# Optimization experiments

Hardware: AMD Instinct MI355X
Metric: run time of the kernel (lower is better)

## Reference

```python
import jax, jax.numpy as jnp
import numpy as np


def setup_inputs() -> dict:
    key = jax.random.key(0)
    ks = jax.random.split(key, 9)
    B, LAT, OBS, HID = 4096, 128, 64, 1024
    s = 0.05  # keep tanh out of full saturation
    return {
        "z": jax.random.normal(ks[0], (B, LAT), jnp.float32),
        "W_l2h": jax.random.normal(ks[1], (HID, LAT), jnp.float32) * s,
        "b_l2h": jax.random.normal(ks[2], (HID,), jnp.float32) * s,
        "W_ih": jax.random.normal(ks[3], (HID, OBS), jnp.float32) * s,
        "b_ih": jax.random.normal(ks[4], (HID,), jnp.float32) * s,
        "W_hh": jax.random.normal(ks[5], (HID, HID), jnp.float32) * s,
        "b_hh": jax.random.normal(ks[6], (HID,), jnp.float32) * s,
        "W_ho": jax.random.normal(ks[7], (OBS, HID), jnp.float32) * s,
        "b_ho": jax.random.normal(ks[8], (OBS,), jnp.float32) * s,
        "seq_len": 70,
    }


def reference(z, W_l2h, b_l2h, W_ih, b_ih, W_hh, b_hh, W_ho, b_ho, seq_len):
    B = z.shape[0]
    obs_dim = W_ho.shape[0]
    # latent -> initial hidden state (nn.Linear)
    h0 = z @ W_l2h.T + b_l2h                         # [B, HID]
    x0 = jnp.zeros((B, obs_dim), dtype=z.dtype)      # first RNN input is zeros

    def step(carry, _):
        h, x = carry
        # tanh RNN cell: h' = tanh(x W_ih^T + b_ih + h W_hh^T + b_hh)
        h = jnp.tanh(x @ W_ih.T + b_ih + h @ W_hh.T + b_hh)
        y = h @ W_ho.T + b_ho                        # output projection [B, OBS]
        x_next = jax.lax.stop_gradient(y)
        return (h, x_next), y

    _, ys = jax.lax.scan(step, (h0, x0), None, length=seq_len)  # [T, B, OBS]
    return jnp.transpose(ys, (1, 0, 2))              # [B, T, OBS]
```

## Files before the change

### kernel.cpp

```cpp
#include <hip/hip_runtime.h>
#include <hip/hip_bf16.h>
#include <stdint.h>

typedef _Float16 f16;
typedef _Float16 f16x8 __attribute__((ext_vector_type(8)));
typedef float f32x4 __attribute__((ext_vector_type(4)));

#define B_SZ 4096
#define HID  1024
#define LAT  128
#define OBS  64
#define TSEQ 70
#define SPLIT_SCALE 2048.0f
#define SPLIT_INV   (1.0f / 2048.0f)

__device__ __forceinline__ size_t tidx(int row, int k, int K) {
  return (size_t)((row >> 4) * (K >> 5) + (k >> 5)) * 512
       + ((k >> 3) & 3) * 128 + (row & 15) * 8 + (k & 7);
}

__device__ __forceinline__ void gl2lds16(const void* g, void* l) {
  __builtin_amdgcn_global_load_lds(
      (const __attribute__((address_space(1))) void*)g,
      (__attribute__((address_space(3))) void*)l, 16, 0, 0);
}

__device__ __forceinline__ float tanh_fast(float x) {
  float e = __expf(2.0f * x);
  return 1.0f - 2.0f / (e + 1.0f);
}

__global__ __launch_bounds__(256, 2) void rnn_step_split(
    const f16* __restrict__ Ah, const f16* __restrict__ Al,
    const f16* __restrict__ Wh, const f16* __restrict__ Wl,
    const float* __restrict__ bias,
    f16* __restrict__ Hh, f16* __restrict__ Hl, int K)
{
  __shared__ __align__(16) f16 ring[3][24 * 512];

  const int lane = threadIdx.x & 63;
  const int wave = threadIdx.x >> 6;
  const int bm = blockIdx.x;
  const int bn = blockIdx.y;
  const int lo8 = lane * 8;
  const int kc = K >> 5;

  f32x4 acc0[2][4], acc1[2][4];
  const f32x4 z4 = {0.f, 0.f, 0.f, 0.f};
#pragma unroll
  for (int i = 0; i < 2; ++i)
#pragma unroll
    for (int j = 0; j < 4; ++j) { acc0[i][j] = z4; acc1[i][j] = z4; }

  auto stage = [&](int it, int slot) {
    f16* b = ring[slot];
#pragma unroll
    for (int u = 0; u < 2; ++u) {
      const int rg = wave * 2 + u;
      const size_t ga = (size_t)((bm * 8 + rg) * kc + it) * 512 + lo8;
      gl2lds16(Ah + ga, b + rg * 512);
      gl2lds16(Al + ga, b + (8 + rg) * 512);
    }
    const size_t gw = (size_t)((bn * 4 + wave) * kc + it) * 512 + lo8;
    gl2lds16(Wh + gw, b + (16 + wave) * 512);
    gl2lds16(Wl + gw, b + (20 + wave) * 512);
  };

  auto compute = [&](int slot) {
    const f16* b = ring[slot];
    f16x8 vah[2], val[2], vwh[4], vwl[4];
#pragma unroll
    for (int i = 0; i < 2; ++i) {
      vah[i] = *(const f16x8*)&b[(wave * 2 + i) * 512 + lo8];
      val[i] = *(const f16x8*)&b[(8 + wave * 2 + i) * 512 + lo8];
    }
#pragma unroll
    for (int j = 0; j < 4; ++j) {
      vwh[j] = *(const f16x8*)&b[(16 + j) * 512 + lo8];
      vwl[j] = *(const f16x8*)&b[(20 + j) * 512 + lo8];
    }
#pragma unroll
    for (int i = 0; i < 2; ++i)
#pragma unroll
      for (int j = 0; j < 4; ++j) {
        acc0[i][j] = __builtin_amdgcn_mfma_f32_16x16x32_f16(vah[i], vwh[j], acc0[i][j], 0, 0, 0);
        acc1[i][j] = __builtin_amdgcn_mfma_f32_16x16x32_f16(vah[i], vwl[j], acc1[i][j], 0, 0, 0);
        acc1[i][j] = __builtin_amdgcn_mfma_f32_16x16x32_f16(val[i], vwh[j], acc1[i][j], 0, 0, 0);
      }
  };

  stage(0, 0);
  int cur = 0;
  for (int it = 0; it + 1 < kc; ++it) {
    const int nxt = (cur == 2) ? 0 : cur + 1;
    stage(it + 1, nxt);
    asm volatile("s_waitcnt vmcnt(6)" ::: "memory");
    __builtin_amdgcn_s_barrier();
    compute(cur);
    cur = nxt;
  }
  asm volatile("s_waitcnt vmcnt(0)" ::: "memory");
  __builtin_amdgcn_s_barrier();
  compute(cur);

  const int rq = lane >> 4;
  const int cl = lane & 15;
#pragma unroll
  for (int j = 0; j < 4; ++j) {
    const int gcol = bn * 64 + j * 16 + cl;
    const float bb = bias[gcol];
#pragma unroll
    for (int i = 0; i < 2; ++i) {
      const int grow = bm * 128 + wave * 32 + i * 16 + rq * 4;
#pragma unroll
      for (int r = 0; r < 4; ++r) {
        const float a = acc0[i][j][r] + acc1[i][j][r] * SPLIT_INV + bb;
        const float t = tanh_fast(a);
        const f16 hi = (f16)t;
        const size_t idx = tidx(grow + r, gcol, HID);
        Hh[idx] = hi;
        Hl[idx] = (f16)((t - (float)hi) * SPLIT_SCALE);
      }
    }
  }
}

__global__ __launch_bounds__(256, 2) void proj_kernel(
    const f16* __restrict__ H, const f16* __restrict__ Who,
    const float* __restrict__ bho, float* __restrict__ Y, int t0)
{
  __shared__ __align__(16) f16 As[128 * 64];
  __shared__ __align__(16) f16 Bs[64 * 64];
  const int lane = threadIdx.x & 63;
  const int wave = threadIdx.x >> 6;
  const int bm = blockIdx.x;
  const int lo8 = lane * 8;

  f32x4 acc[2][4];
  const f32x4 z4 = {0.f, 0.f, 0.f, 0.f};
#pragma unroll
  for (int i = 0; i < 2; ++i)
#pragma unroll
    for (int j = 0; j < 4; ++j) acc[i][j] = z4;

  for (int kt = 0; kt < HID; kt += 64) {
    const int kch = kt >> 5;
#pragma unroll
    for (int u = 0; u < 4; ++u) {
      const int cidx = wave * 4 + u;
      const int mt = cidx >> 1, s = cidx & 1;
      gl2lds16(H + (size_t)((bm * 8 + mt) * 32 + kch + s) * 512 + lo8, &As[cidx * 512]);
    }
#pragma unroll
    for (int u = 0; u < 2; ++u) {
      const int cidx = wave * 2 + u;
      const int nt = cidx >> 1, s = cidx & 1;
      gl2lds16(Who + (size_t)(nt * 32 + kch + s) * 512 + lo8, &Bs[cidx * 512]);
    }
    __syncthreads();
#pragma unroll
    for (int s = 0; s < 2; ++s) {
      f16x8 af[2], bfr[4];
#pragma unroll
      for (int i = 0; i < 2; ++i)
        af[i] = *(const f16x8*)&As[(((wave * 2 + i) << 1) | s) * 512 + lo8];
#pragma unroll
      for (int j = 0; j < 4; ++j)
        bfr[j] = *(const f16x8*)&Bs[((j << 1) | s) * 512 + lo8];
#pragma unroll
      for (int i = 0; i < 2; ++i)
#pragma unroll
        for (int j = 0; j < 4; ++j)
          acc[i][j] = __builtin_amdgcn_mfma_f32_16x16x32_f16(af[i], bfr[j], acc[i][j], 0, 0, 0);
    }
    __syncthreads();
  }

  const int rq = lane >> 4;
  const int cl = lane & 15;
#pragma unroll
  for (int j = 0; j < 4; ++j) {
    const int col = j * 16 + cl;
    const float bb = bho[col];
#pragma unroll
    for (int i = 0; i < 2; ++i)
#pragma unroll
      for (int r = 0; r < 4; ++r) {
        const int row = bm * 128 + wave * 32 + i * 16 + rq * 4 + r;
        const int t = t0 + (row >> 12);
        const int b = row & 4095;
        Y[((size_t)b * TSEQ + t) * OBS + col] = acc[i][j][r] + bb;
      }
  }
}

__global__ void cast_tiled_kernel(const float* __restrict__ x, f16* __restrict__ y,
                                  int K, int n) {
  int i = blockIdx.x * blockDim.x + threadIdx.x;
  if (i < n) y[tidx(i / K, i % K, K)] = (f16)x[i];
}

__global__ void split_tiled_kernel(const float* __restrict__ x, f16* __restrict__ hi,
                                   f16* __restrict__ lo, int K, int n) {
  int i = blockIdx.x * blockDim.x + threadIdx.x;
  if (i < n) {
    float v = x[i];
    f16 h = (f16)v;
    size_t o = tidx(i / K, i % K, K);
    hi[o] = h;
    lo[o] = (f16)((v - (float)h) * SPLIT_SCALE);
  }
}

__global__ void prep_weff(const float* __restrict__ Whh, const float* __restrict__ Wih,
                          const float* __restrict__ Who,
                          f16* __restrict__ Wh, f16* __restrict__ Wl) {
  const int n = blockIdx.x;
  __shared__ float wih_row[OBS];
  if (threadIdx.x < OBS) wih_row[threadIdx.x] = Wih[n * OBS + threadIdx.x];
  __syncthreads();
  for (int k = threadIdx.x; k < HID; k += 256) {
    float s = Whh[(size_t)n * HID + k];
#pragma unroll 8
    for (int o = 0; o < OBS; ++o) s = fmaf(wih_row[o], Who[(size_t)o * HID + k], s);
    const size_t idx = tidx(n, k, HID);
    f16 h = (f16)s;
    Wh[idx] = h;
    Wl[idx] = (f16)((s - (float)h) * SPLIT_SCALE);
  }
}

__global__ void prep_w1(const float* __restrict__ Whh, const float* __restrict__ Wl2h,
                        f16* __restrict__ W1h, f16* __restrict__ W1l) {
  const int n = blockIdx.x, j = threadIdx.x;
  float s = 0.f;
  for (int k = 0; k < HID; ++k) s = fmaf(Whh[(size_t)n * HID + k], Wl2h[(size_t)k * LAT + j], s);
  const size_t idx = tidx(n, j, LAT);
  f16 h = (f16)s;
  W1h[idx] = h;
  W1l[idx] = (f16)((s - (float)h) * SPLIT_SCALE);
}

__global__ void prep_bias(const float* __restrict__ bih, const float* __restrict__ bhh,
                          const float* __restrict__ bho, const float* __restrict__ Wih,
                          const float* __restrict__ Whh, const float* __restrict__ bl2h,
                          float* __restrict__ beff, float* __restrict__ b1) {
  const int n = blockIdx.x, l = threadIdx.x;
  float s1 = Wih[(size_t)n * OBS + l] * bho[l];
  float s2 = 0.f;
  for (int k = l; k < HID; k += 64) s2 = fmaf(Whh[(size_t)n * HID + k], bl2h[k], s2);
#pragma unroll
  for (int off = 32; off > 0; off >>= 1) {
    s1 += __shfl_down(s1, off);
    s2 += __shfl_down(s2, off);
  }
  if (l == 0) {
    const float base = bih[n] + bhh[n];
    beff[n] = base + s1;
    b1[n]   = base + s2;
  }
}

extern "C" void kernel_launch(void* const* d_in, const int* in_sizes, int n_in,
                              void* d_out, int out_size, void* d_ws, size_t ws_size,
                              hipStream_t stream) {
  (void)in_sizes; (void)n_in; (void)out_size; (void)ws_size;
  const float* z    = (const float*)d_in[0];
  const float* Wl2h = (const float*)d_in[1];
  const float* bl2h = (const float*)d_in[2];
  const float* Wih  = (const float*)d_in[3];
  const float* bih  = (const float*)d_in[4];
  const float* Whh  = (const float*)d_in[5];
  const float* bhh  = (const float*)d_in[6];
  const float* Who  = (const float*)d_in[7];
  const float* bho  = (const float*)d_in[8];
  float* Y = (float*)d_out;

  char* ws = (char*)d_ws;
  size_t off = 0;
  auto take = [&](size_t bytes) {
    char* p = ws + off;
    off = (off + bytes + 255) & ~(size_t)255;
    return p;
  };
  f16*   Weffh = (f16*)take((size_t)HID * HID * 2);
  f16*   Weffl = (f16*)take((size_t)HID * HID * 2);
  f16*   W1h   = (f16*)take((size_t)HID * LAT * 2);
  f16*   W1l   = (f16*)take((size_t)HID * LAT * 2);
  f16*   Whob  = (f16*)take((size_t)OBS * HID * 2);
  f16*   zh    = (f16*)take((size_t)B_SZ * LAT * 2);
  f16*   zl    = (f16*)take((size_t)B_SZ * LAT * 2);
  float* beff  = (float*)take(HID * 4);
  float* b1    = (float*)take(HID * 4);

  const size_t S = (size_t)B_SZ * HID;
  f16* Hlo  = (f16*)take(2 * S * 2);
  f16* ring = (f16*)take(8 * S * 2);

  split_tiled_kernel<<<(B_SZ * LAT) / 256, 256, 0, stream>>>(z, zh, zl, LAT, B_SZ * LAT);
  cast_tiled_kernel<<<(OBS * HID) / 256, 256, 0, stream>>>(Who, Whob, HID, OBS * HID);
  prep_weff<<<HID, 256, 0, stream>>>(Whh, Wih, Who, Weffh, Weffl);
  prep_w1<<<HID, LAT, 0, stream>>>(Whh, Wl2h, W1h, W1l);
  prep_bias<<<HID, 64, 0, stream>>>(bih, bhh, bho, Wih, Whh, bl2h, beff, b1);

  dim3 sgrid(B_SZ / 128, HID / 64);
  rnn_step_split<<<sgrid, 256, 0, stream>>>(zh, zl, W1h, W1l, b1, ring, Hlo, LAT);
  for (int t = 1; t < TSEQ; ++t) {
    if ((t & 7) == 0)
      proj_kernel<<<(8 * B_SZ) / 128, 256, 0, stream>>>(ring, Whob, bho, Y, t - 8);
    rnn_step_split<<<sgrid, 256, 0, stream>>>(
        ring + (size_t)((t - 1) & 7) * S, Hlo + (size_t)((t - 1) & 1) * S,
        Weffh, Weffl, beff,
        ring + (size_t)(t & 7) * S, Hlo + (size_t)(t & 1) * S, HID);
  }
  proj_kernel<<<(6 * B_SZ) / 128, 256, 0, stream>>>(ring, Whob, bho, Y, 64);
}
```

Measured before the change: 2.180 ms.

## Load A fragments directly into registers, stage only weights through LDS ring

```diff
diff --git a/kernel.cpp b/kernel.cpp
--- a/kernel.cpp
+++ b/kernel.cpp
@@ -36,7 +36,7 @@
     const float* __restrict__ bias,
     f16* __restrict__ Hh, f16* __restrict__ Hl, int K)
 {
-  __shared__ __align__(16) f16 ring[3][24 * 512];
+  __shared__ __align__(16) f16 ringW[3][8 * 512];
 
   const int lane = threadIdx.x & 63;
   const int wave = threadIdx.x >> 6;
@@ -52,56 +52,74 @@
 #pragma unroll
     for (int j = 0; j < 4; ++j) { acc0[i][j] = z4; acc1[i][j] = z4; }
 
-  auto stage = [&](int it, int slot) {
-    f16* b = ring[slot];
-#pragma unroll
-    for (int u = 0; u < 2; ++u) {
-      const int rg = wave * 2 + u;
-      const size_t ga = (size_t)((bm * 8 + rg) * kc + it) * 512 + lo8;
-      gl2lds16(Ah + ga, b + rg * 512);
-      gl2lds16(Al + ga, b + (8 + rg) * 512);
+  const size_t aRow0 = (size_t)(bm * 8 + wave * 2) * kc;
+  const size_t aRow1 = aRow0 + kc;
+
+  struct ABuf { f16x8 h0, h1, l0, l1; };
+  auto loadA = [&](int it, ABuf& A) {
+    A.h0 = *(const f16x8*)(Ah + (aRow0 + it) * 512 + lo8);
+    A.l0 = *(const f16x8*)(Al + (aRow0 + it) * 512 + lo8);
+    A.h1 = *(const f16x8*)(Ah + (aRow1 + it) * 512 + lo8);
+    A.l1 = *(const f16x8*)(Al + (aRow1 + it) * 512 + lo8);
+  };
+
+  auto stageW = [&](int it, int slot) {
+    f16* b = ringW[slot];
+    const size_t gw = (size_t)((bn * 4 + wave) * kc + it) * 512 + lo8;
+    gl2lds16(Wh + gw, b + wave * 512);
+    gl2lds16(Wl + gw, b + (4 + wave) * 512);
+  };
+
+  auto compute = [&](int slot, const ABuf& A) {
+    const f16* b = ringW[slot];
+    f16x8 vwh[4], vwl[4];
+#pragma unroll
+    for (int j = 0; j < 4; ++j) {
+      vwh[j] = *(const f16x8*)&b[j * 512 + lo8];
+      vwl[j] = *(const f16x8*)&b[(4 + j) * 512 + lo8];
     }
-    const size_t gw = (size_t)((bn * 4 + wave) * kc + it) * 512 + lo8;
-    gl2lds16(Wh + gw, b + (16 + wave) * 512);
-    gl2lds16(Wl + gw, b + (20 + wave) * 512);
-  };
-
-  auto compute = [&](int slot) {
-    const f16* b = ring[slot];
-    f16x8 vah[2], val[2], vwh[4], vwl[4];
-#pragma unroll
-    for (int i = 0; i < 2; ++i) {
-      vah[i] = *(const f16x8*)&b[(wave * 2 + i) * 512 + lo8];
-      val[i] = *(const f16x8*)&b[(8 + wave * 2 + i) * 512 + lo8];
+#pragma unroll
+    for (int j = 0; j < 4; ++j) {
+      acc0[0][j] = __builtin_amdgcn_mfma_f32_16x16x32_f16(A.h0, vwh[j], acc0[0][j], 0, 0, 0);
+      acc1[0][j] = __builtin_amdgcn_mfma_f32_16x16x32_f16(A.h0, vwl[j], acc1[0][j], 0, 0, 0);
+      acc1[0][j] = __builtin_amdgcn_mfma_f32_16x16x32_f16(A.l0, vwh[j], acc1[0][j], 0, 0, 0);
+      acc0[1][j] = __builtin_amdgcn_mfma_f32_16x16x32_f16(A.h1, vwh[j], acc0[1][j], 0, 0, 0);
+      acc1[1][j] = __builtin_amdgcn_mfma_f32_16x16x32_f16(A.h1, vwl[j], acc1[1][j], 0, 0, 0);
+      acc1[1][j] = __builtin_amdgcn_mfma_f32_16x16x32_f16(A.l1, vwh[j], acc1[1][j], 0, 0, 0);
     }
-#pragma unroll
-    for (int j = 0; j < 4; ++j) {
-      vwh[j] = *(const f16x8*)&b[(16 + j) * 512 + lo8];
-      vwl[j] = *(const f16x8*)&b[(20 + j) * 512 + lo8];
-    }
-#pragma unroll
-    for (int i = 0; i < 2; ++i)
-#pragma unroll
-      for (int j = 0; j < 4; ++j) {
-        acc0[i][j] = __builtin_amdgcn_mfma_f32_16x16x32_f16(vah[i], vwh[j], acc0[i][j], 0, 0, 0);
-        acc1[i][j] = __builtin_amdgcn_mfma_f32_16x16x32_f16(vah[i], vwl[j], acc1[i][j], 0, 0, 0);
-        acc1[i][j] = __builtin_amdgcn_mfma_f32_16x16x32_f16(val[i], vwh[j], acc1[i][j], 0, 0, 0);
-      }
-  };
-
-  stage(0, 0);
-  int cur = 0;
-  for (int it = 0; it + 1 < kc; ++it) {
-    const int nxt = (cur == 2) ? 0 : cur + 1;
-    stage(it + 1, nxt);
+  };
+
+  ABuf A0, A1;
+  loadA(0, A0);
+  stageW(0, 0);
+  int s0 = 0;
+  int it = 0;
+  for (; it + 2 < kc; it += 2) {
+    const int s1 = (s0 == 2) ? 0 : s0 + 1;
+    const int s2 = (s1 == 2) ? 0 : s1 + 1;
+    loadA(it + 1, A1);
+    stageW(it + 1, s1);
     asm volatile("s_waitcnt vmcnt(6)" ::: "memory");
     __builtin_amdgcn_s_barrier();
-    compute(cur);
-    cur = nxt;
-  }
-  asm volatile("s_waitcnt vmcnt(0)" ::: "memory");
-  __builtin_amdgcn_s_barrier();
-  compute(cur);
+    compute(s0, A0);
+    loadA(it + 2, A0);
+    stageW(it + 2, s2);
+    asm volatile("s_waitcnt vmcnt(6)" ::: "memory");
+    __builtin_amdgcn_s_barrier();
+    compute(s1, A1);
+    s0 = s2;
+  }
+  {
+    const int s1 = (s0 == 2) ? 0 : s0 + 1;
+    loadA(kc - 1, A1);
+    stageW(kc - 1, s1);
+    asm volatile("s_waitcnt vmcnt(6)" ::: "memory");
+    __builtin_amdgcn_s_barrier();
+    compute(s0, A0);
+    asm volatile("s_waitcnt vmcnt(0)" ::: "memory");
+    __builtin_amdgcn_s_barrier();
+    compute(s1, A1);
+  }
 
   const int rq = lane >> 4;
   const int cl = lane & 15;
@@ -129,12 +147,12 @@
     const f16* __restrict__ H, const f16* __restrict__ Who,
     const float* __restrict__ bho, float* __restrict__ Y, int t0)
 {
-  __shared__ __align__(16) f16 As[128 * 64];
-  __shared__ __align__(16) f16 Bs[64 * 64];
+  __shared__ __align__(16) f16 ringB[3][4 * 512];
   const int lane = threadIdx.x & 63;
   const int wave = threadIdx.x >> 6;
   const int bm = blockIdx.x;
   const int lo8 = lane * 8;
+  const int kc = HID >> 5;
 
   f32x4 acc[2][4];
   const f32x4 z4 = {0.f, 0.f, 0.f, 0.f};
@@ -143,37 +161,59 @@
 #pragma unroll
     for (int j = 0; j < 4; ++j) acc[i][j] = z4;
 
-  for (int kt = 0; kt < HID; kt += 64) {
-    const int kch = kt >> 5;
-#pragma unroll
-    for (int u = 0; u < 4; ++u) {
-      const int cidx = wave * 4 + u;
-      const int mt = cidx >> 1, s = cidx & 1;
-      gl2lds16(H + (size_t)((bm * 8 + mt) * 32 + kch + s) * 512 + lo8, &As[cidx * 512]);
+  const size_t aRow0 = (size_t)(bm * 8 + wave * 2) * kc;
+  const size_t aRow1 = aRow0 + kc;
+
+  struct ABuf { f16x8 a0, a1; };
+  auto loadA = [&](int it, ABuf& A) {
+    A.a0 = *(const f16x8*)(H + (aRow0 + it) * 512 + lo8);
+    A.a1 = *(const f16x8*)(H + (aRow1 + it) * 512 + lo8);
+  };
+  auto stageB = [&](int it, int slot) {
+    gl2lds16(Who + (size_t)(wave * kc + it) * 512 + lo8, ringB[slot] + wave * 512);
+  };
+  auto compute = [&](int slot, const ABuf& A) {
+    const f16* b = ringB[slot];
+    f16x8 bf[4];
+#pragma unroll
+    for (int j = 0; j < 4; ++j) bf[j] = *(const f16x8*)&b[j * 512 + lo8];
+#pragma unroll
+    for (int j = 0; j < 4; ++j) {
+      acc[0][j] = __builtin_amdgcn_mfma_f32_16x16x32_f16(A.a0, bf[j], acc[0][j], 0, 0, 0);
+      acc[1][j] = __builtin_amdgcn_mfma_f32_16x16x32_f16(A.a1, bf[j], acc[1][j], 0, 0, 0);
     }
-#pragma unroll
-    for (int u = 0; u < 2; ++u) {
-      const int cidx = wave * 2 + u;
-      const int nt = cidx >> 1, s = cidx & 1;
-      gl2lds16(Who + (size_t)(nt * 32 + kch + s) * 512 + lo8, &Bs[cidx * 512]);
-    }
-    __syncthreads();
-#pragma unroll
-    for (int s = 0; s < 2; ++s) {
-      f16x8 af[2], bfr[4];
-#pragma unroll
-      for (int i = 0; i < 2; ++i)
-        af[i] = *(const f16x8*)&As[(((wave * 2 + i) << 1) | s) * 512 + lo8];
-#pragma unroll
-      for (int j = 0; j < 4; ++j)
-        bfr[j] = *(const f16x8*)&Bs[((j << 1) | s) * 512 + lo8];
-#pragma unroll
-      for (int i = 0; i < 2; ++i)
-#pragma unroll
-        for (int j = 0; j < 4; ++j)
-          acc[i][j] = __builtin_amdgcn_mfma_f32_16x16x32_f16(af[i], bfr[j], acc[i][j], 0, 0, 0);
-    }
-    __syncthreads();
+  };
+
+  ABuf A0, A1;
+  loadA(0, A0);
+  stageB(0, 0);
+  int s0 = 0;
+  int it = 0;
+  for (; it + 2 < kc; it += 2) {
+    const int s1 = (s0 == 2) ? 0 : s0 + 1;
+    const int s2 = (s1 == 2) ? 0 : s1 + 1;
+    loadA(it + 1, A1);
+    stageB(it + 1, s1);
+    asm volatile("s_waitcnt vmcnt(3)" ::: "memory");
+    __builtin_amdgcn_s_barrier();
+    compute(s0, A0);
+    loadA(it + 2, A0);
+    stageB(it + 2, s2);
+    asm volatile("s_waitcnt vmcnt(3)" ::: "memory");
+    __builtin_amdgcn_s_barrier();
+    compute(s1, A1);
+    s0 = s2;
+  }
+  {
+    const int s1 = (s0 == 2) ? 0 : s0 + 1;
+    loadA(kc - 1, A1);
+    stageB(kc - 1, s1);
+    asm volatile("s_waitcnt vmcnt(3)" ::: "memory");
+    __builtin_amdgcn_s_barrier();
+    compute(s0, A0);
+    asm volatile("s_waitcnt vmcnt(0)" ::: "memory");
+    __builtin_amdgcn_s_barrier();
+    compute(s1, A1);
   }
 
   const int rq = lane >> 4;
```

Measured after the change: 2.373 ms. 1.09x slower.

## Add weight-resident LDS kernel for recurrent steps with 512x32 tiles

Applied to the files above, without the earlier changes.

```diff
diff --git a/kernel.cpp b/kernel.cpp
--- a/kernel.cpp
+++ b/kernel.cpp
@@ -28,6 +28,102 @@
 __device__ __forceinline__ float tanh_fast(float x) {
   float e = __expf(2.0f * x);
   return 1.0f - 2.0f / (e + 1.0f);
+}
+
+__global__ __launch_bounds__(256, 1) void rnn_step_wres(
+    const f16* __restrict__ Ah, const f16* __restrict__ Al,
+    const f16* __restrict__ Wh, const f16* __restrict__ Wl,
+    const float* __restrict__ bias,
+    f16* __restrict__ Hh, f16* __restrict__ Hl)
+{
+  extern __shared__ __align__(16) f16 sW[];
+  const int lane = threadIdx.x & 63;
+  const int wave = threadIdx.x >> 6;
+  const int rb = blockIdx.x & 7;
+  const int cb = blockIdx.x >> 3;
+  const int lo8 = lane * 8;
+  const int kcA = 32;
+
+#pragma unroll
+  for (int u = 0; u < 32; ++u) {
+    const int g = wave * 32 + u;
+    const f16* src = (g < 64) ? Wh : Wl;
+    const int nrg = (g & 63) >> 5, kcid = g & 31;
+    gl2lds16(src + ((size_t)((cb * 2 + nrg) * 32 + kcid)) * 512 + lo8,
+             sW + g * 512);
+  }
+
+  f32x4 acc0[8][2], acc1[8][2];
+  const f32x4 z4 = {0.f, 0.f, 0.f, 0.f};
+#pragma unroll
+  for (int r = 0; r < 8; ++r)
+#pragma unroll
+    for (int j = 0; j < 2; ++j) { acc0[r][j] = z4; acc1[r][j] = z4; }
+
+  const int rgbase = rb * 32 + wave * 8;
+
+  struct ABuf { f16x8 h[8], l[8]; };
+  auto loadA = [&](int it, ABuf& A) {
+#pragma unroll
+    for (int r = 0; r < 8; ++r) {
+      const size_t ga = ((size_t)(rgbase + r) * kcA + it) * 512 + lo8;
+      A.h[r] = *(const f16x8*)(Ah + ga);
+      A.l[r] = *(const f16x8*)(Al + ga);
+    }
+  };
+
+  auto compute = [&](int it, const ABuf& A) {
+    f16x8 vwh[2], vwl[2];
+#pragma unroll
+    for (int j = 0; j < 2; ++j) {
+      vwh[j] = *(const f16x8*)&sW[(j * 32 + it) * 512 + lo8];
+      vwl[j] = *(const f16x8*)&sW[(64 + j * 32 + it) * 512 + lo8];
+    }
+#pragma unroll
+    for (int r = 0; r < 8; ++r)
+#pragma unroll
+      for (int j = 0; j < 2; ++j) {
+        acc0[r][j] = __builtin_amdgcn_mfma_f32_16x16x32_f16(A.h[r], vwh[j], acc0[r][j], 0, 0, 0);
+        acc1[r][j] = __builtin_amdgcn_mfma_f32_16x16x32_f16(A.h[r], vwl[j], acc1[r][j], 0, 0, 0);
+        acc1[r][j] = __builtin_amdgcn_mfma_f32_16x16x32_f16(A.l[r], vwh[j], acc1[r][j], 0, 0, 0);
+      }
+  };
+
+  ABuf A0, A1;
+  loadA(0, A0);
+  __syncthreads();
+
+  int it = 0;
+  for (; it + 2 < kcA; it += 2) {
+    loadA(it + 1, A1);
+    compute(it, A0);
+    loadA(it + 2, A0);
+    compute(it + 1, A1);
+  }
+  loadA(kcA - 1, A1);
+  compute(kcA - 2, A0);
+  compute(kcA - 1, A1);
+
+  const int rq = lane >> 4;
+  const int cl = lane & 15;
+#pragma unroll
+  for (int j = 0; j < 2; ++j) {
+    const int gcol = cb * 32 + j * 16 + cl;
+    const float bb = bias[gcol];
+#pragma unroll
+    for (int r = 0; r < 8; ++r) {
+      const int grow = rb * 512 + wave * 128 + r * 16 + rq * 4;
+#pragma unroll
+      for (int rr = 0; rr < 4; ++rr) {
+        const float a = acc0[r][j][rr] + acc1[r][j][rr] * SPLIT_INV + bb;
+        const float t = tanh_fast(a);
+        const f16 hi = (f16)t;
+        const size_t idx = tidx(grow + rr, gcol, HID);
+        Hh[idx] = hi;
+        Hl[idx] = (f16)((t - (float)hi) * SPLIT_SCALE);
+      }
+    }
+  }
 }
 
 __global__ __launch_bounds__(256, 2) void rnn_step_split(
@@ -275,6 +371,13 @@
   const float* Who  = (const float*)d_in[7];
   const float* bho  = (const float*)d_in[8];
   float* Y = (float*)d_out;
+
+  static bool configured = false;
+  if (!configured) {
+    hipFuncSetAttribute(reinterpret_cast<const void*>(rnn_step_wres),
+                        hipFuncAttributeMaxDynamicSharedMemorySize, 131072);
+    configured = true;
+  }
 
   char* ws = (char*)d_ws;
   size_t off = 0;
@@ -308,10 +411,10 @@
   for (int t = 1; t < TSEQ; ++t) {
     if ((t & 7) == 0)
       proj_kernel<<<(8 * B_SZ) / 128, 256, 0, stream>>>(ring, Whob, bho, Y, t - 8);
-    rnn_step_split<<<sgrid, 256, 0, stream>>>(
+    rnn_step_wres<<<256, 256, 131072, stream>>>(
         ring + (size_t)((t - 1) & 7) * S, Hlo + (size_t)((t - 1) & 1) * S,
         Weffh, Weffl, beff,
-        ring + (size_t)(t & 7) * S, Hlo + (size_t)(t & 1) * S, HID);
+        ring + (size_t)(t & 7) * S, Hlo + (size_t)(t & 1) * S);
   }
   proj_kernel<<<(6 * B_SZ) / 128, 256, 0, stream>>>(ring, Whob, bho, Y, 64);
 }
```

Measured after the change: 5.951 ms. +173.0%, slower.

## Fuse output projection of previous step into the recurrent step kernel

Applied to the files above, without the earlier changes.

```diff
diff --git a/kernel.cpp b/kernel.cpp
--- a/kernel.cpp
+++ b/kernel.cpp
@@ -34,9 +34,11 @@
     const f16* __restrict__ Ah, const f16* __restrict__ Al,
     const f16* __restrict__ Wh, const f16* __restrict__ Wl,
     const float* __restrict__ bias,
-    f16* __restrict__ Hh, f16* __restrict__ Hl, int K)
+    f16* __restrict__ Hh, f16* __restrict__ Hl, int K,
+    const f16* __restrict__ Who, const float* __restrict__ bho,
+    float* __restrict__ Y, int t_prev)
 {
-  __shared__ __align__(16) f16 ring[3][24 * 512];
+  __shared__ __align__(16) f16 ring[3][25 * 512];
 
   const int lane = threadIdx.x & 63;
   const int wave = threadIdx.x >> 6;
@@ -44,13 +46,16 @@
   const int bn = blockIdx.y;
   const int lo8 = lane * 8;
   const int kc = K >> 5;
-
-  f32x4 acc0[2][4], acc1[2][4];
+  const bool doproj = (t_prev >= 0) && (bn < 4);
+
+  f32x4 acc0[2][4], acc1[2][4], accy[2];
   const f32x4 z4 = {0.f, 0.f, 0.f, 0.f};
 #pragma unroll
-  for (int i = 0; i < 2; ++i)
+  for (int i = 0; i < 2; ++i) {
 #pragma unroll
     for (int j = 0; j < 4; ++j) { acc0[i][j] = z4; acc1[i][j] = z4; }
+    accy[i] = z4;
+  }
 
   auto stage = [&](int it, int slot) {
     f16* b = ring[slot];
@@ -64,6 +69,13 @@
     const size_t gw = (size_t)((bn * 4 + wave) * kc + it) * 512 + lo8;
     gl2lds16(Wh + gw, b + (16 + wave) * 512);
     gl2lds16(Wl + gw, b + (20 + wave) * 512);
+    if (doproj && wave == 0)
+      gl2lds16(Who + (size_t)(bn * 32 + it) * 512 + lo8, b + 24 * 512);
+  };
+
+  auto waitPrev = [&]() {
+    if (doproj && wave == 0) asm volatile("s_waitcnt vmcnt(7)" ::: "memory");
+    else                     asm volatile("s_waitcnt vmcnt(6)" ::: "memory");
   };
 
   auto compute = [&](int slot) {
@@ -87,6 +99,11 @@
         acc1[i][j] = __builtin_amdgcn_mfma_f32_16x16x32_f16(vah[i], vwl[j], acc1[i][j], 0, 0, 0);
         acc1[i][j] = __builtin_amdgcn_mfma_f32_16x16x32_f16(val[i], vwh[j], acc1[i][j], 0, 0, 0);
       }
+    if (doproj) {
+      const f16x8 vwho = *(const f16x8*)&b[24 * 512 + lo8];
+      accy[0] = __builtin_amdgcn_mfma_f32_16x16x32_f16(vah[0], vwho, accy[0], 0, 0, 0);
+      accy[1] = __builtin_amdgcn_mfma_f32_16x16x32_f16(vah[1], vwho, accy[1], 0, 0, 0);
+    }
   };
 
   stage(0, 0);
@@ -94,7 +111,7 @@
   for (int it = 0; it + 1 < kc; ++it) {
     const int nxt = (cur == 2) ? 0 : cur + 1;
     stage(it + 1, nxt);
-    asm volatile("s_waitcnt vmcnt(6)" ::: "memory");
+    waitPrev();
     __builtin_amdgcn_s_barrier();
     compute(cur);
     cur = nxt;
@@ -122,6 +139,17 @@
         Hl[idx] = (f16)((t - (float)hi) * SPLIT_SCALE);
       }
     }
+  }
+  if (doproj) {
+    const int ycol = bn * 16 + cl;
+    const float yb = bho[ycol];
+#pragma unroll
+    for (int i = 0; i < 2; ++i)
+#pragma unroll
+      for (int r = 0; r < 4; ++r) {
+        const int brow = bm * 128 + wave * 32 + i * 16 + rq * 4 + r;
+        Y[((size_t)brow * TSEQ + t_prev) * OBS + ycol] = accy[i][r] + yb;
+      }
   }
 }
 
@@ -295,7 +323,7 @@
 
   const size_t S = (size_t)B_SZ * HID;
   f16* Hlo  = (f16*)take(2 * S * 2);
-  f16* ring = (f16*)take(8 * S * 2);
+  f16* Hhi  = (f16*)take(2 * S * 2);
 
   split_tiled_kernel<<<(B_SZ * LAT) / 256, 256, 0, stream>>>(z, zh, zl, LAT, B_SZ * LAT);
   cast_tiled_kernel<<<(OBS * HID) / 256, 256, 0, stream>>>(Who, Whob, HID, OBS * HID);
@@ -304,14 +332,14 @@
   prep_bias<<<HID, 64, 0, stream>>>(bih, bhh, bho, Wih, Whh, bl2h, beff, b1);
 
   dim3 sgrid(B_SZ / 128, HID / 64);
-  rnn_step_split<<<sgrid, 256, 0, stream>>>(zh, zl, W1h, W1l, b1, ring, Hlo, LAT);
+  rnn_step_split<<<sgrid, 256, 0, stream>>>(zh, zl, W1h, W1l, b1,
+      Hhi, Hlo, LAT, nullptr, nullptr, nullptr, -1);
   for (int t = 1; t < TSEQ; ++t) {
-    if ((t & 7) == 0)
-      proj_kernel<<<(8 * B_SZ) / 128, 256, 0, stream>>>(ring, Whob, bho, Y, t - 8);
     rnn_step_split<<<sgrid, 256, 0, stream>>>(
-        ring + (size_t)((t - 1) & 7) * S, Hlo + (size_t)((t - 1) & 1) * S,
+        Hhi + (size_t)((t - 1) & 1) * S, Hlo + (size_t)((t - 1) & 1) * S,
         Weffh, Weffl, beff,
-        ring + (size_t)(t & 7) * S, Hlo + (size_t)(t & 1) * S, HID);
-  }
-  proj_kernel<<<(6 * B_SZ) / 128, 256, 0, stream>>>(ring, Whob, bho, Y, 64);
-}
+        Hhi + (size_t)(t & 1) * S, Hlo + (size_t)(t & 1) * S, HID,
+        Whob, bho, Y, t - 1);
+  }
+  proj_kernel<<<32, 256, 0, stream>>>(Hhi + S, Whob, bho, Y, 69);
+}
```

New measurement: 2.233 ms. 2.4% more time.
